# Kernel optimization log

Measured on AMD Instinct MI355X. Metric: run time of the kernel, lower is better.

The kernel has to match this reference:

```python
import jax, jax.numpy as jnp
import numpy as np

B, D, T = 4, 1024, 512      # z: [B, input_dim, T]
V, CD = 32000, 4096          # codebook: [codebook_size, codebook_dim]
EPS = 1e-12                  # F.normalize default eps


def setup_inputs() -> dict:
    key = jax.random.key(0)
    k1, k2, k3, k4 = jax.random.split(key, 4)
    z = jax.random.normal(k1, (B, D, T), dtype=jnp.float32)
    codebook = jax.random.normal(k2, (V, CD), dtype=jnp.float32) * 0.02
    cb_w = jax.random.normal(k3, (D, CD), dtype=jnp.float32) * 0.02  # torch Linear weight [out,in]
    cb_b = jax.random.normal(k4, (D,), dtype=jnp.float32) * 0.02
    return {"z": z, "codebook": codebook, "cb_w": cb_w, "cb_b": cb_b}


def _l2norm(x):
    n = jnp.sqrt(jnp.sum(x * x, axis=1, keepdims=True))
    return x / jnp.maximum(n, EPS)


def reference(z, codebook, cb_w, cb_b):
    # stride == 1, use_cblinear == True -> z_e = z
    z_e = z                                              # [B, D, T]
    proj_cb = codebook @ cb_w.T + cb_b                    # [V, D] cb_proj(codebook)

    # decode_latents
    enc = jnp.transpose(z_e, (0, 2, 1)).reshape(-1, D)    # (B*T, D)
    enc_n = _l2norm(enc)
    cb_n = _l2norm(proj_cb)
    dist = (jnp.sum(enc_n * enc_n, axis=1, keepdims=True)
            - 2.0 * enc_n @ cb_n.T
            + jnp.sum(cb_n * cb_n, axis=1)[None, :])      # (B*T, V)
    indices = jnp.argmax(-dist, axis=1).reshape(B, T)     # argmin distance
    z_q = jnp.transpose(proj_cb[indices], (0, 2, 1))      # gather un-normalized codes -> [B, D, T]

    commitment_loss = jnp.mean((z_e - jax.lax.stop_gradient(z_q)) ** 2, axis=(1, 2))  # [B]
    codebook_loss = jnp.mean((z_q - jax.lax.stop_gradient(z_e)) ** 2, axis=(1, 2))    # [B]
    z_q_st = z_e + jax.lax.stop_gradient(z_q - z_e)       # straight-through
    return z_q_st, indices, commitment_loss, codebook_loss
```

## Files before the change

### kernel.cpp

```cpp
#include <hip/hip_runtime.h>
#include <hip/hip_bf16.h>
#include <math.h>

#define B_  4
#define D_  1024
#define T_  512
#define V_  32000
#define CD_ 4096
#define NR  (B_*T_)
#define VT2 (V_/256)

typedef __attribute__((ext_vector_type(8))) short short8v;
typedef __attribute__((ext_vector_type(4))) float f32x4;

#define MFMA16(a,b,c) __builtin_amdgcn_mfma_f32_16x16x32_bf16((a),(b),(c),0,0,0)

#define ASM_VMCNT0() asm volatile("s_waitcnt vmcnt(0)" ::: "memory")
#define ASM_LGKM0()  asm volatile("s_waitcnt lgkmcnt(0)" ::: "memory")
#define SCHED_BAR()  __builtin_amdgcn_sched_barrier(0)

__device__ __forceinline__ unsigned short f2bf(float f) {
    return __builtin_bit_cast(unsigned short, __float2bfloat16(f));
}
__device__ __forceinline__ float bf2f(unsigned short u) {
    unsigned int v = ((unsigned int)u) << 16;
    return __builtin_bit_cast(float, v);
}
__device__ __forceinline__ void glds16(const unsigned short* g, unsigned short* l) {
    __builtin_amdgcn_global_load_lds(
        (const __attribute__((address_space(1))) unsigned int*)g,
        (__attribute__((address_space(3))) unsigned int*)l, 16, 0, 0);
}
__device__ __forceinline__ void cvt8(const float4& x, const float4& y,
                                     short8v& h, short8v& l) {
    float xs[8] = {x.x, x.y, x.z, x.w, y.x, y.y, y.z, y.w};
    #pragma unroll
    for (int e = 0; e < 8; ++e) {
        unsigned short hb = f2bf(xs[e]);
        h[e] = (short)hb;
        l[e] = (short)f2bf(xs[e] - bf2f(hb));
    }
}
__device__ __forceinline__ int xcd_swz(int wg, int nwg) {
    int q = nwg >> 3, r = nwg & 7;
    int x = wg & 7, o = wg >> 3;
    return (x < r ? x * (q + 1) : r * (q + 1) + (x - r) * q) + o;
}

__global__ __launch_bounds__(256) void vq_cvt(const float* __restrict__ x,
                                              unsigned short* __restrict__ hi,
                                              unsigned short* __restrict__ lo,
                                              size_t n4) {
    size_t stride = (size_t)gridDim.x * 256;
    for (size_t i = (size_t)blockIdx.x * 256 + threadIdx.x; i < n4; i += stride) {
        float4 v = *(const float4*)(x + 4 * i);
        float xs[4] = {v.x, v.y, v.z, v.w};
        ushort4 h, l;
        unsigned short* hp = (unsigned short*)&h;
        unsigned short* lp = (unsigned short*)&l;
        #pragma unroll
        for (int e = 0; e < 4; ++e) {
            hp[e] = f2bf(xs[e]);
            lp[e] = f2bf(xs[e] - bf2f(hp[e]));
        }
        *(ushort4*)(hi + 4 * i) = h;
        *(ushort4*)(lo + 4 * i) = l;
    }
}

#define T8_PHASE(pp, EXTRA)                                                   \
    {                                                                         \
        short8v aAh = *(const short8v*)&smem[cur][0][(wr8 + 2*(pp)) * 512 + lane8];     \
        short8v aAl = *(const short8v*)&smem[cur][1][(wr8 + 2*(pp)) * 512 + lane8];     \
        short8v aBh = *(const short8v*)&smem[cur][0][(wr8 + 2*(pp) + 1) * 512 + lane8]; \
        short8v aBl = *(const short8v*)&smem[cur][1][(wr8 + 2*(pp) + 1) * 512 + lane8]; \
        EXTRA;                                                                \
        SCHED_BAR();                                                          \
        __builtin_amdgcn_s_barrier();                                         \
        ASM_LGKM0();                                                          \
        SCHED_BAR();                                                          \
        __builtin_amdgcn_s_setprio(1);                                        \
        _Pragma("unroll")                                                     \
        for (int nf = 0; nf < 4; ++nf) {                                      \
            acc[2*(pp)][nf]   = MFMA16(aAh, bh[nf], acc[2*(pp)][nf]);         \
            acc[2*(pp)][nf]   = MFMA16(aAh, bl[nf], acc[2*(pp)][nf]);         \
            acc[2*(pp)][nf]   = MFMA16(aAl, bh[nf], acc[2*(pp)][nf]);         \
            acc[2*(pp)+1][nf] = MFMA16(aBh, bh[nf], acc[2*(pp)+1][nf]);       \
            acc[2*(pp)+1][nf] = MFMA16(aBh, bl[nf], acc[2*(pp)+1][nf]);       \
            acc[2*(pp)+1][nf] = MFMA16(aBl, bh[nf], acc[2*(pp)+1][nf]);       \
        }                                                                     \
        __builtin_amdgcn_s_setprio(0);                                        \
        __builtin_amdgcn_s_barrier();                                         \
        SCHED_BAR();                                                          \
    }

#define T8_CORE(KD)                                                           \
    f32x4 acc[8][4];                                                          \
    _Pragma("unroll")                                                         \
    for (int i = 0; i < 8; ++i)                                               \
        _Pragma("unroll")                                                     \
        for (int j = 0; j < 4; ++j) acc[i][j] = (f32x4){0.f, 0.f, 0.f, 0.f};  \
    const int lane = threadIdx.x & 63, w = threadIdx.x >> 6;                  \
    const int wr = w >> 2, wc = w & 3;                                        \
    const int r16 = lane & 15, kg = lane >> 4;                                \
    const int lane8 = lane * 8, wr8 = wr * 8, wc4 = wc * 4;                   \
    const int pw = w >> 1;                                                    \
    const unsigned short* gplane = (pw == 0) ? Ahp : (pw == 1) ? Alp          \
                                   : (pw == 2) ? Bhp : Blp;                   \
    const int baseRow = (pw < 2 ? mt : nt) + (w & 1) * 128 + r16;             \
    const unsigned short* gsrc = gplane + (size_t)baseRow * (KD) + kg * 8;    \
    unsigned short* lb0 = &smem[0][pw][(w & 1) * 4096 + lane8];               \
    unsigned short* lb1 = &smem[1][pw][(w & 1) * 4096 + lane8];               \
    _Pragma("unroll")                                                         \
    for (int q = 0; q < 8; ++q)                                               \
        glds16(gsrc + (size_t)q * 16 * (KD), lb0 + q * 512);                  \
    ASM_VMCNT0();                                                             \
    __builtin_amdgcn_s_barrier();                                             \
    SCHED_BAR();                                                              \
    const int NT = (KD) / 32;                                                 \
    for (int t = 0; t < NT; ++t) {                                            \
        const int cur = t & 1;                                                \
        unsigned short* lbN = cur ? lb0 : lb1;                                \
        short8v bh[4], bl[4];                                                 \
        _Pragma("unroll")                                                     \
        for (int nf = 0; nf < 4; ++nf) {                                      \
            bh[nf] = *(const short8v*)&smem[cur][2][(wc4 + nf) * 512 + lane8];\
            bl[nf] = *(const short8v*)&smem[cur][3][(wc4 + nf) * 512 + lane8];\
        }                                                                     \
        T8_PHASE(0,                                                           \
            if (t + 1 < NT) {                                                 \
                const size_t kof = (size_t)(t + 1) * 32;                      \
                _Pragma("unroll")                                             \
                for (int q = 0; q < 8; ++q)                                   \
                    glds16(gsrc + kof + (size_t)q * 16 * (KD), lbN + q * 512);\
            })                                                                \
        T8_PHASE(1, (void)0)                                                  \
        T8_PHASE(2, (void)0)                                                  \
        T8_PHASE(3, if (t + 1 < NT) { ASM_VMCNT0(); })                        \
    }

__global__ __launch_bounds__(512, 2) void vq_gemm1_t8(
    const unsigned short* __restrict__ Ahp, const unsigned short* __restrict__ Alp,
    const unsigned short* __restrict__ Bhp, const unsigned short* __restrict__ Blp,
    const float* __restrict__ bias,
    unsigned short* __restrict__ Phi, unsigned short* __restrict__ Plo)
{
    __shared__ unsigned short smem[2][4][8192];
    const int wg = xcd_swz(blockIdx.x, (V_/256) * (D_/256));
    const int mt = (wg >> 2) * 256;
    const int nt = (wg & 3) * 256;

    T8_CORE(CD_)

    #pragma unroll
    for (int nf = 0; nf < 4; ++nf) {
        const int col = nt + wc * 64 + nf * 16 + r16;
        const float bv = bias[col];
        #pragma unroll
        for (int mf = 0; mf < 8; ++mf) {
            const int rbase = mt + wr * 128 + mf * 16 + kg * 4;
            #pragma unroll
            for (int r = 0; r < 4; ++r) {
                float vv = acc[mf][nf][r] + bv;
                unsigned short h = f2bf(vv);
                unsigned short l = f2bf(vv - bf2f(h));
                size_t o = (size_t)(rbase + r) * D_ + col;
                Phi[o] = h; Plo[o] = l;
            }
        }
    }
}

__global__ __launch_bounds__(512, 2) void vq_gemm2_t8(
    const unsigned short* __restrict__ Ahp, const unsigned short* __restrict__ Alp,
    const unsigned short* __restrict__ Bhp, const unsigned short* __restrict__ Blp,
    const float* __restrict__ ninv,
    float* __restrict__ pmax, int* __restrict__ pidx)
{
    __shared__ unsigned short smem[2][4][8192];
    const int wg = xcd_swz(blockIdx.x, (NR/256) * VT2);
    const int nid = wg >> 3;
    const int mt = (wg & 7) * 256;
    const int nt = nid * 256;

    T8_CORE(D_)

    float* redv = (float*)&smem[0][0][0];
    int*   redi = (int*)&smem[0][0][2048];
    float nv[4];
    #pragma unroll
    for (int nf = 0; nf < 4; ++nf) nv[nf] = ninv[nt + wc * 64 + nf * 16 + r16];
    #pragma unroll
    for (int mf = 0; mf < 8; ++mf) {
        #pragma unroll
        for (int r = 0; r < 4; ++r) {
            float best = -INFINITY; int bi = 0x7fffffff;
            #pragma unroll
            for (int nf = 0; nf < 4; ++nf) {
                float v = acc[mf][nf][r] * nv[nf];
                int ci = nt + wc * 64 + nf * 16 + r16;
                if (v > best || (v == best && ci < bi)) { best = v; bi = ci; }
            }
            #pragma unroll
            for (int m = 8; m >= 1; m >>= 1) {
                float ov = __shfl_xor(best, m, 16);
                int   oi = __shfl_xor(bi,   m, 16);
                if (ov > best || (ov == best && oi < bi)) { best = ov; bi = oi; }
            }
            if (r16 == 0) {
                int rl = wr * 128 + mf * 16 + kg * 4 + r;
                redv[rl * 4 + wc] = best; redi[rl * 4 + wc] = bi;
            }
        }
    }
    __builtin_amdgcn_s_barrier();
    if (threadIdx.x < 256) {
        float best = -INFINITY; int bi = 0x7fffffff;
        #pragma unroll
        for (int c = 0; c < 4; ++c) {
            float v = redv[threadIdx.x * 4 + c];
            int   i = redi[threadIdx.x * 4 + c];
            if (v > best || (v == best && i < bi)) { best = v; bi = i; }
        }
        size_t o = (size_t)(mt + threadIdx.x) * VT2 + nid;
        pmax[o] = best; pidx[o] = bi;
    }
}

__global__ __launch_bounds__(256) void vq_gemm1_mfma(
    const float* __restrict__ A,
    const unsigned short* __restrict__ Bhi, const unsigned short* __restrict__ Blo,
    const float* __restrict__ bias,
    unsigned short* __restrict__ Phi, unsigned short* __restrict__ Plo)
{
    __shared__ unsigned short smem[2][4][4096];
    const int tid = threadIdx.x;
    const int lane = tid & 63, w = tid >> 6;
    const int wr = w >> 1, wc = w & 1;
    const int m_tile = blockIdx.y * 128;
    const int n_tile = blockIdx.x * 128;
    const int row16 = lane & 15, kg = lane >> 4;
    const int s0 = 2 * w, s1 = s0 + 1;
    const int lane8 = lane * 8, wr4 = wr * 4, wc4 = wc * 4;

    const float*          Ap0 = A   + (size_t)(m_tile + s0*16 + row16) * CD_ + kg*8;
    const float*          Ap1 = A   + (size_t)(m_tile + s1*16 + row16) * CD_ + kg*8;
    const unsigned short* Bp0 = Bhi + (size_t)(n_tile + s0*16 + row16) * CD_ + kg*8;
    const unsigned short* Bp1 = Bhi + (size_t)(n_tile + s1*16 + row16) * CD_ + kg*8;
    const unsigned short* Lp0 = Blo + (size_t)(n_tile + s0*16 + row16) * CD_ + kg*8;
    const unsigned short* Lp1 = Blo + (size_t)(n_tile + s1*16 + row16) * CD_ + kg*8;

    f32x4 acc[4][4];
    #pragma unroll
    for (int i = 0; i < 4; ++i)
        #pragma unroll
        for (int j = 0; j < 4; ++j) acc[i][j] = (f32x4){0.f, 0.f, 0.f, 0.f};

    float4 aw[4], al_[4];
    aw[0] = *(const float4*)(Ap0);     aw[1] = *(const float4*)(Ap0 + 4);
    aw[2] = *(const float4*)(Ap1);     aw[3] = *(const float4*)(Ap1 + 4);
    glds16(Bp0, (unsigned short*)&smem[0][2][s0*512]);
    glds16(Bp1, (unsigned short*)&smem[0][2][s1*512]);
    glds16(Lp0, (unsigned short*)&smem[0][3][s0*512]);
    glds16(Lp1, (unsigned short*)&smem[0][3][s1*512]);
    {
        short8v h0, l0, h1, l1;
        cvt8(aw[0], aw[1], h0, l0);
        cvt8(aw[2], aw[3], h1, l1);
        *(short8v*)&smem[0][0][s0*512 + lane8] = h0;
        *(short8v*)&smem[0][1][s0*512 + lane8] = l0;
        *(short8v*)&smem[0][0][s1*512 + lane8] = h1;
        *(short8v*)&smem[0][1][s1*512 + lane8] = l1;
    }
    aw[0] = *(const float4*)(Ap0 + 32); aw[1] = *(const float4*)(Ap0 + 36);
    aw[2] = *(const float4*)(Ap1 + 32); aw[3] = *(const float4*)(Ap1 + 36);
    __syncthreads();

    int cur = 0;
    const int NT = CD_ / 32;
    for (int t = 0; t < NT; ++t) {
        if (t + 1 < NT) {
            const size_t ko = (size_t)(t + 1) * 32;
            glds16(Bp0 + ko, (unsigned short*)&smem[cur^1][2][s0*512]);
            glds16(Bp1 + ko, (unsigned short*)&smem[cur^1][2][s1*512]);
            glds16(Lp0 + ko, (unsigned short*)&smem[cur^1][3][s0*512]);
            glds16(Lp1 + ko, (unsigned short*)&smem[cur^1][3][s1*512]);
            short8v h0, l0, h1, l1;
            cvt8(aw[0], aw[1], h0, l0);
            cvt8(aw[2], aw[3], h1, l1);
            *(short8v*)&smem[cur^1][0][s0*512 + lane8] = h0;
            *(short8v*)&smem[cur^1][1][s0*512 + lane8] = l0;
            *(short8v*)&smem[cur^1][0][s1*512 + lane8] = h1;
            *(short8v*)&smem[cur^1][1][s1*512 + lane8] = l1;
        }
        if (t + 2 < NT) {
            const size_t ko2 = (size_t)(t + 2) * 32;
            al_[0] = *(const float4*)(Ap0 + ko2);  al_[1] = *(const float4*)(Ap0 + ko2 + 4);
            al_[2] = *(const float4*)(Ap1 + ko2);  al_[3] = *(const float4*)(Ap1 + ko2 + 4);
        }
        short8v ah[4], av[4], bh[4], bl[4];
        #pragma unroll
        for (int f = 0; f < 4; ++f) {
            ah[f] = *(const short8v*)&smem[cur][0][(wr4+f)*512 + lane8];
            av[f] = *(const short8v*)&smem[cur][1][(wr4+f)*512 + lane8];
            bh[f] = *(const short8v*)&smem[cur][2][(wc4+f)*512 + lane8];
            bl[f] = *(const short8v*)&smem[cur][3][(wc4+f)*512 + lane8];
        }
        #pragma unroll
        for (int mf = 0; mf < 4; ++mf)
            #pragma unroll
            for (int nf = 0; nf < 4; ++nf) {
                acc[mf][nf] = MFMA16(ah[mf], bh[nf], acc[mf][nf]);
                acc[mf][nf] = MFMA16(ah[mf], bl[nf], acc[mf][nf]);
                acc[mf][nf] = MFMA16(av[mf], bh[nf], acc[mf][nf]);
            }
        __syncthreads();
        #pragma unroll
        for (int q = 0; q < 4; ++q) aw[q] = al_[q];
        cur ^= 1;
    }

    #pragma unroll
    for (int nf = 0; nf < 4; ++nf) {
        const int col = n_tile + wc*64 + nf*16 + row16;
        const float bv = bias[col];
        #pragma unroll
        for (int mf = 0; mf < 4; ++mf) {
            const int rbase = m_tile + wr*64 + mf*16 + kg*4;
            #pragma unroll
            for (int r = 0; r < 4; ++r) {
                float vv = acc[mf][nf][r] + bv;
                unsigned short h = f2bf(vv);
                unsigned short l = f2bf(vv - bf2f(h));
                size_t o = (size_t)(rbase + r) * D_ + col;
                Phi[o] = h; Plo[o] = l;
            }
        }
    }
}

__global__ __launch_bounds__(256) void vq_norms_pl(const unsigned short* __restrict__ ph,
                                                   const unsigned short* __restrict__ pl,
                                                   float* __restrict__ ninv) {
    const int row  = blockIdx.x * 4 + (threadIdx.x >> 6);
    const int lane = threadIdx.x & 63;
    float s = 0.f;
    #pragma unroll
    for (int q = 0; q < 2; ++q) {
        size_t o = (size_t)row * D_ + q * 512 + lane * 8;
        short8v h = *(const short8v*)(ph + o);
        short8v l = *(const short8v*)(pl + o);
        #pragma unroll
        for (int e = 0; e < 8; ++e) {
            float x = bf2f((unsigned short)h[e]) + bf2f((unsigned short)l[e]);
            s += x * x;
        }
    }
    #pragma unroll
    for (int off = 32; off >= 1; off >>= 1) s += __shfl_down(s, off);
    if (lane == 0) ninv[row] = 1.0f / fmaxf(sqrtf(s), 1e-12f);
}

__global__ __launch_bounds__(256) void vq_transpose_cvt(const float* __restrict__ z,
                                                        unsigned short* __restrict__ ehi,
                                                        unsigned short* __restrict__ elo) {
    __shared__ float tile[64][65];
    const int b = blockIdx.z, t0 = blockIdx.x * 64, d0 = blockIdx.y * 64;
    const int lane = threadIdx.x & 63, sub = threadIdx.x >> 6;
    for (int dd = sub; dd < 64; dd += 4)
        tile[dd][lane] = z[((size_t)b * D_ + d0 + dd) * T_ + t0 + lane];
    __syncthreads();
    for (int tt = sub; tt < 64; tt += 4) {
        float v = tile[lane][tt];
        unsigned short h = f2bf(v);
        unsigned short l = f2bf(v - bf2f(h));
        size_t o = (size_t)(b * T_ + t0 + tt) * D_ + d0 + lane;
        ehi[o] = h; elo[o] = l;
    }
}

__global__ __launch_bounds__(256) void vq_argmerge(const float* __restrict__ pmax,
                                                   const int* __restrict__ pidx,
                                                   int* __restrict__ idxw,
                                                   float* __restrict__ outI,
                                                   int vt) {
    const int i = blockIdx.x * 256 + threadIdx.x;
    if (i >= NR) return;
    float best = -INFINITY; int bi = 0;
    for (int c = 0; c < vt; c++) {
        float v = pmax[(size_t)i * vt + c];
        int   ii = pidx[(size_t)i * vt + c];
        if (v > best || (v == best && ii < bi)) { best = v; bi = ii; }
    }
    idxw[i] = bi;
    outI[i] = (float)bi;
}

__global__ __launch_bounds__(256) void vq_gather_pl(const unsigned short* __restrict__ ph,
                                                    const unsigned short* __restrict__ pl,
                                                    const int* __restrict__ idxw,
                                                    const float* __restrict__ z,
                                                    float* __restrict__ out0,
                                                    float* __restrict__ lpart) {
    __shared__ float zq[64][65];
    __shared__ int idx_s[64];
    __shared__ float wsum[4];
    const int b = blockIdx.z, t0 = blockIdx.x * 64, d0 = blockIdx.y * 64;
    const int tid = threadIdx.x;
    const int lane = tid & 63, sub = tid >> 6;
    if (tid < 64) idx_s[tid] = idxw[b * T_ + t0 + tid];
    __syncthreads();
    for (int tt = sub; tt < 64; tt += 4) {
        size_t o = (size_t)idx_s[tt] * D_ + d0 + lane;
        zq[tt][lane] = bf2f(ph[o]) + bf2f(pl[o]);
    }
    __syncthreads();
    float lacc = 0.f;
    for (int dd = sub; dd < 64; dd += 4) {
        const size_t base = ((size_t)b * D_ + d0 + dd) * T_ + t0 + lane;
        float q = zq[lane][dd];
        float zv = z[base];
        out0[base] = q;
        float dv = zv - q;
        lacc += dv * dv;
    }
    #pragma unroll
    for (int off = 32; off >= 1; off >>= 1) lacc += __shfl_down(lacc, off);
    if (lane == 0) wsum[sub] = lacc;
    __syncthreads();
    if (tid == 0)
        lpart[(blockIdx.z * 16 + blockIdx.y) * 8 + blockIdx.x] =
            wsum[0] + wsum[1] + wsum[2] + wsum[3];
}

__global__ void vq_loss(const float* __restrict__ lpart, float* __restrict__ outL) {
    const int b = threadIdx.x;
    if (b >= B_) return;
    float s = 0.f;
    for (int q = 0; q < 128; q++) s += lpart[b * 128 + q];
    s /= (float)(D_ * T_);
    outL[b]      = s;
    outL[B_ + b] = s;
}

extern "C" void kernel_launch(void* const* d_in, const int* in_sizes, int n_in,
                              void* d_out, int out_size, void* d_ws, size_t ws_size,
                              hipStream_t stream) {
    const float* z        = (const float*)d_in[0];
    const float* codebook = (const float*)d_in[1];
    const float* cb_w     = (const float*)d_in[2];
    const float* cb_b     = (const float*)d_in[3];

    float* out0 = (float*)d_out;
    float* outI = out0 + (size_t)B_*D_*T_;
    float* outL = outI + NR;

    char* p = (char*)d_ws;
    auto alloc = [&](size_t bytes) { char* r = p; p += (bytes + 255) & ~(size_t)255; return r; };
    unsigned short* w_hi = (unsigned short*)alloc((size_t)D_ * CD_ * 2);
    unsigned short* w_lo = (unsigned short*)alloc((size_t)D_ * CD_ * 2);
    unsigned short* p_hi = (unsigned short*)alloc((size_t)V_ * D_ * 2);
    unsigned short* p_lo = (unsigned short*)alloc((size_t)V_ * D_ * 2);
    unsigned short* e_hi = (unsigned short*)alloc((size_t)NR * D_ * 2);
    unsigned short* e_lo = (unsigned short*)alloc((size_t)NR * D_ * 2);
    float* ninv  = (float*)alloc((size_t)V_ * 4);
    float* pmax  = (float*)alloc((size_t)NR * VT2 * 4);
    int*   pidx  = (int*)  alloc((size_t)NR * VT2 * 4);
    int*   idxw  = (int*)  alloc((size_t)NR * 4);
    float* lpart = (float*)alloc((size_t)2048 * 4);
    unsigned short* c_hi = (unsigned short*)alloc((size_t)V_ * CD_ * 2);
    unsigned short* c_lo = (unsigned short*)alloc((size_t)V_ * CD_ * 2);
    size_t need_full = (size_t)(p - (char*)d_ws);

    vq_cvt<<<1024, 256, 0, stream>>>(cb_w, w_hi, w_lo, (size_t)D_ * CD_ / 4);
    vq_transpose_cvt<<<dim3(T_/64, D_/64, B_), 256, 0, stream>>>(z, e_hi, e_lo);

    if (ws_size >= need_full) {
        vq_cvt<<<4096, 256, 0, stream>>>(codebook, c_hi, c_lo, (size_t)V_ * CD_ / 4);
        vq_gemm1_t8<<<(V_/256) * (D_/256), 512, 0, stream>>>(c_hi, c_lo, w_hi, w_lo,
                                                             cb_b, p_hi, p_lo);
    } else {
        vq_gemm1_mfma<<<dim3(D_/128, V_/128), 256, 0, stream>>>(codebook, w_hi, w_lo,
                                                                cb_b, p_hi, p_lo);
    }
    vq_norms_pl<<<V_/4, 256, 0, stream>>>(p_hi, p_lo, ninv);
    vq_gemm2_t8<<<(NR/256) * VT2, 512, 0, stream>>>(e_hi, e_lo, p_hi, p_lo,
                                                    ninv, pmax, pidx);
    vq_argmerge<<<NR/256, 256, 0, stream>>>(pmax, pidx, idxw, outI, VT2);
    vq_gather_pl<<<dim3(T_/64, D_/64, B_), 256, 0, stream>>>(p_hi, p_lo, idxw, z,
                                                             out0, lpart);
    vq_loss<<<1, 64, 0, stream>>>(lpart, outL);
}
```

Baseline: 1.546 ms.

## Shrink both split-bf16 GEMMs to 128x128 tiles with simpler double-buffered loop

```diff
diff --git a/kernel.cpp b/kernel.cpp
--- a/kernel.cpp
+++ b/kernel.cpp
@@ -8,13 +8,14 @@
 #define V_  32000
 #define CD_ 4096
 #define NR  (B_*T_)
-#define VT2 (V_/256)
+#define VT  (V_/128)
 
 typedef __attribute__((ext_vector_type(8))) short short8v;
 typedef __attribute__((ext_vector_type(4))) float f32x4;
 
 #define MFMA16(a,b,c) __builtin_amdgcn_mfma_f32_16x16x32_bf16((a),(b),(c),0,0,0)
 
+#define ASM_VMCNT4() asm volatile("s_waitcnt vmcnt(4)" ::: "memory")
 #define ASM_VMCNT0() asm volatile("s_waitcnt vmcnt(0)" ::: "memory")
 #define ASM_LGKM0()  asm volatile("s_waitcnt lgkmcnt(0)" ::: "memory")
 #define SCHED_BAR()  __builtin_amdgcn_sched_barrier(0)
@@ -68,97 +69,102 @@
     }
 }
 
-#define T8_PHASE(pp, EXTRA)                                                   \
-    {                                                                         \
-        short8v aAh = *(const short8v*)&smem[cur][0][(wr8 + 2*(pp)) * 512 + lane8];     \
-        short8v aAl = *(const short8v*)&smem[cur][1][(wr8 + 2*(pp)) * 512 + lane8];     \
-        short8v aBh = *(const short8v*)&smem[cur][0][(wr8 + 2*(pp) + 1) * 512 + lane8]; \
-        short8v aBl = *(const short8v*)&smem[cur][1][(wr8 + 2*(pp) + 1) * 512 + lane8]; \
-        EXTRA;                                                                \
-        SCHED_BAR();                                                          \
-        __builtin_amdgcn_s_barrier();                                         \
-        ASM_LGKM0();                                                          \
-        SCHED_BAR();                                                          \
-        __builtin_amdgcn_s_setprio(1);                                        \
-        _Pragma("unroll")                                                     \
-        for (int nf = 0; nf < 4; ++nf) {                                      \
-            acc[2*(pp)][nf]   = MFMA16(aAh, bh[nf], acc[2*(pp)][nf]);         \
-            acc[2*(pp)][nf]   = MFMA16(aAh, bl[nf], acc[2*(pp)][nf]);         \
-            acc[2*(pp)][nf]   = MFMA16(aAl, bh[nf], acc[2*(pp)][nf]);         \
-            acc[2*(pp)+1][nf] = MFMA16(aBh, bh[nf], acc[2*(pp)+1][nf]);       \
-            acc[2*(pp)+1][nf] = MFMA16(aBh, bl[nf], acc[2*(pp)+1][nf]);       \
-            acc[2*(pp)+1][nf] = MFMA16(aBl, bh[nf], acc[2*(pp)+1][nf]);       \
-        }                                                                     \
-        __builtin_amdgcn_s_setprio(0);                                        \
-        __builtin_amdgcn_s_barrier();                                         \
-        SCHED_BAR();                                                          \
-    }
-
-#define T8_CORE(KD)                                                           \
-    f32x4 acc[8][4];                                                          \
+#define W128_CORE(KD)                                                         \
+    f32x4 acc[2][4];                                                          \
     _Pragma("unroll")                                                         \
-    for (int i = 0; i < 8; ++i)                                               \
+    for (int i = 0; i < 2; ++i)                                               \
         _Pragma("unroll")                                                     \
         for (int j = 0; j < 4; ++j) acc[i][j] = (f32x4){0.f, 0.f, 0.f, 0.f};  \
     const int lane = threadIdx.x & 63, w = threadIdx.x >> 6;                  \
-    const int wr = w >> 2, wc = w & 3;                                        \
+    const int wr = w >> 1, wc = w & 1;                                        \
     const int r16 = lane & 15, kg = lane >> 4;                                \
-    const int lane8 = lane * 8, wr8 = wr * 8, wc4 = wc * 4;                   \
-    const int pw = w >> 1;                                                    \
-    const unsigned short* gplane = (pw == 0) ? Ahp : (pw == 1) ? Alp          \
-                                   : (pw == 2) ? Bhp : Blp;                   \
-    const int baseRow = (pw < 2 ? mt : nt) + (w & 1) * 128 + r16;             \
-    const unsigned short* gsrc = gplane + (size_t)baseRow * (KD) + kg * 8;    \
-    unsigned short* lb0 = &smem[0][pw][(w & 1) * 4096 + lane8];               \
-    unsigned short* lb1 = &smem[1][pw][(w & 1) * 4096 + lane8];               \
+    const int lane8 = lane * 8;                                               \
+    const unsigned short* gs[4];                                              \
+    unsigned short* lds0[4];                                                  \
+    unsigned short* lds1[4];                                                  \
     _Pragma("unroll")                                                         \
-    for (int q = 0; q < 8; ++q)                                               \
-        glds16(gsrc + (size_t)q * 16 * (KD), lb0 + q * 512);                  \
+    for (int q = 0; q < 4; ++q) {                                             \
+        const int u = w * 4 + q;                                              \
+        const int pl = u >> 3, sub = u & 7;                                   \
+        const unsigned short* gp = (pl == 0) ? Ahp : (pl == 1) ? Alp          \
+                                   : (pl == 2) ? Bhp : Blp;                   \
+        const int row = ((pl < 2) ? mt : nt) + sub * 16 + r16;                \
+        gs[q] = gp + (size_t)row * (KD) + kg * 8;                             \
+        lds0[q] = &smem[0][pl][sub * 512 + lane8];                            \
+        lds1[q] = &smem[1][pl][sub * 512 + lane8];                            \
+    }                                                                         \
+    _Pragma("unroll")                                                         \
+    for (int q = 0; q < 4; ++q) glds16(gs[q], lds0[q]);                       \
     ASM_VMCNT0();                                                             \
     __builtin_amdgcn_s_barrier();                                             \
     SCHED_BAR();                                                              \
     const int NT = (KD) / 32;                                                 \
     for (int t = 0; t < NT; ++t) {                                            \
         const int cur = t & 1;                                                \
-        unsigned short* lbN = cur ? lb0 : lb1;                                \
-        short8v bh[4], bl[4];                                                 \
+        if (t + 1 < NT) {                                                     \
+            const size_t kof = (size_t)(t + 1) * 32;                          \
+            _Pragma("unroll")                                                 \
+            for (int q = 0; q < 4; ++q)                                       \
+                glds16(gs[q] + kof, cur ? lds0[q] : lds1[q]);                 \
+            ASM_VMCNT4();       \
+        } else {                                                              \
+            ASM_VMCNT0();                                                     \
+        }                                                                     \
+        __builtin_amdgcn_s_barrier();                                         \
+        SCHED_BAR();                                                          \
+        short8v ah[2], al[2], bh[4], bl[4];                                   \
+        _Pragma("unroll")                                                     \
+        for (int mf = 0; mf < 2; ++mf) {                                      \
+            ah[mf] = *(const short8v*)&smem[cur][0][(wr*2 + mf)*512 + lane8]; \
+            al[mf] = *(const short8v*)&smem[cur][1][(wr*2 + mf)*512 + lane8]; \
+        }                                                                     \
         _Pragma("unroll")                                                     \
         for (int nf = 0; nf < 4; ++nf) {                                      \
-            bh[nf] = *(const short8v*)&smem[cur][2][(wc4 + nf) * 512 + lane8];\
-            bl[nf] = *(const short8v*)&smem[cur][3][(wc4 + nf) * 512 + lane8];\
+            bh[nf] = *(const short8v*)&smem[cur][2][(wc*4 + nf)*512 + lane8]; \
+            bl[nf] = *(const short8v*)&smem[cur][3][(wc*4 + nf)*512 + lane8]; \
         }                                                                     \
-        T8_PHASE(0,                                                           \
-            if (t + 1 < NT) {                                                 \
-                const size_t kof = (size_t)(t + 1) * 32;                      \
-                _Pragma("unroll")                                             \
-                for (int q = 0; q < 8; ++q)                                   \
-                    glds16(gsrc + kof + (size_t)q * 16 * (KD), lbN + q * 512);\
-            })                                                                \
-        T8_PHASE(1, (void)0)                                                  \
-        T8_PHASE(2, (void)0)                                                  \
-        T8_PHASE(3, if (t + 1 < NT) { ASM_VMCNT0(); })                        \
-    }
-
-__global__ __launch_bounds__(512, 2) void vq_gemm1_t8(
+        __builtin_amdgcn_s_setprio(1);                                        \
+        _Pragma("unroll")                                                     \
+        for (int mf = 0; mf < 2; ++mf)                                        \
+            _Pragma("unroll")                                                 \
+            for (int nf = 0; nf < 4; ++nf)                                    \
+                acc[mf][nf] = MFMA16(ah[mf], bh[nf], acc[mf][nf]);            \
+        _Pragma("unroll")                                                     \
+        for (int mf = 0; mf < 2; ++mf)                                        \
+            _Pragma("unroll")                                                 \
+            for (int nf = 0; nf < 4; ++nf)                                    \
+                acc[mf][nf] = MFMA16(ah[mf], bl[nf], acc[mf][nf]);            \
+        _Pragma("unroll")                                                     \
+        for (int mf = 0; mf < 2; ++mf)                                        \
+            _Pragma("unroll")                                                 \
+            for (int nf = 0; nf < 4; ++nf)                                    \
+                acc[mf][nf] = MFMA16(al[mf], bh[nf], acc[mf][nf]);            \
+        __builtin_amdgcn_s_setprio(0);                                        \
+        ASM_LGKM0();                                                          \
+        __builtin_amdgcn_s_barrier();                                         \
+        SCHED_BAR();                                                          \
+    }
+
+__global__ __launch_bounds__(512, 4) void vq_gemm1_w(
     const unsigned short* __restrict__ Ahp, const unsigned short* __restrict__ Alp,
     const unsigned short* __restrict__ Bhp, const unsigned short* __restrict__ Blp,
     const float* __restrict__ bias,
     unsigned short* __restrict__ Phi, unsigned short* __restrict__ Plo)
 {
-    __shared__ unsigned short smem[2][4][8192];
-    const int wg = xcd_swz(blockIdx.x, (V_/256) * (D_/256));
-    const int mt = (wg >> 2) * 256;
-    const int nt = (wg & 3) * 256;
-
-    T8_CORE(CD_)
+    __shared__ unsigned short smem[2][4][4096];
+    const int wg = xcd_swz(blockIdx.x, VT * (D_/128));
+    const int mt = (wg >> 3) * 128;
+    const int nt = (wg & 7) * 128;
+
+    W128_CORE(CD_)
 
     #pragma unroll
     for (int nf = 0; nf < 4; ++nf) {
         const int col = nt + wc * 64 + nf * 16 + r16;
         const float bv = bias[col];
         #pragma unroll
-        for (int mf = 0; mf < 8; ++mf) {
-            const int rbase = mt + wr * 128 + mf * 16 + kg * 4;
+        for (int mf = 0; mf < 2; ++mf) {
+            const int rbase = mt + wr * 32 + mf * 16 + kg * 4;
             #pragma unroll
             for (int r = 0; r < 4; ++r) {
                 float vv = acc[mf][nf][r] + bv;
@@ -171,27 +177,27 @@
     }
 }
 
-__global__ __launch_bounds__(512, 2) void vq_gemm2_t8(
+__global__ __launch_bounds__(512, 4) void vq_gemm2_w(
     const unsigned short* __restrict__ Ahp, const unsigned short* __restrict__ Alp,
     const unsigned short* __restrict__ Bhp, const unsigned short* __restrict__ Blp,
     const float* __restrict__ ninv,
     float* __restrict__ pmax, int* __restrict__ pidx)
 {
-    __shared__ unsigned short smem[2][4][8192];
-    const int wg = xcd_swz(blockIdx.x, (NR/256) * VT2);
-    const int nid = wg >> 3;
-    const int mt = (wg & 7) * 256;
-    const int nt = nid * 256;
-
-    T8_CORE(D_)
+    __shared__ unsigned short smem[2][4][4096];
+    const int wg = xcd_swz(blockIdx.x, (NR/128) * VT);
+    const int nid = wg >> 4;
+    const int mt = (wg & 15) * 128;
+    const int nt = nid * 128;
+
+    W128_CORE(D_)
 
     float* redv = (float*)&smem[0][0][0];
-    int*   redi = (int*)&smem[0][0][2048];
+    int*   redi = (int*)&smem[0][0][1024];
     float nv[4];
     #pragma unroll
     for (int nf = 0; nf < 4; ++nf) nv[nf] = ninv[nt + wc * 64 + nf * 16 + r16];
     #pragma unroll
-    for (int mf = 0; mf < 8; ++mf) {
+    for (int mf = 0; mf < 2; ++mf) {
         #pragma unroll
         for (int r = 0; r < 4; ++r) {
             float best = -INFINITY; int bi = 0x7fffffff;
@@ -208,22 +214,19 @@
                 if (ov > best || (ov == best && oi < bi)) { best = ov; bi = oi; }
             }
             if (r16 == 0) {
-                int rl = wr * 128 + mf * 16 + kg * 4 + r;
-                redv[rl * 4 + wc] = best; redi[rl * 4 + wc] = bi;
+                int rl = wr * 32 + mf * 16 + kg * 4 + r;
+                redv[wc * 128 + rl] = best; redi[wc * 128 + rl] = bi;
             }
         }
     }
     __builtin_amdgcn_s_barrier();
-    if (threadIdx.x < 256) {
-        float best = -INFINITY; int bi = 0x7fffffff;
-        #pragma unroll
-        for (int c = 0; c < 4; ++c) {
-            float v = redv[threadIdx.x * 4 + c];
-            int   i = redi[threadIdx.x * 4 + c];
-            if (v > best || (v == best && i < bi)) { best = v; bi = i; }
-        }
-        size_t o = (size_t)(mt + threadIdx.x) * VT2 + nid;
-        pmax[o] = best; pidx[o] = bi;
+    if (threadIdx.x < 128) {
+        float v0 = redv[threadIdx.x],       v1 = redv[128 + threadIdx.x];
+        int   i0 = redi[threadIdx.x],       i1 = redi[128 + threadIdx.x];
+        bool t1 = (v1 > v0) || (v1 == v0 && i1 < i0);
+        size_t o = (size_t)(mt + threadIdx.x) * VT + nid;
+        pmax[o] = t1 ? v1 : v0;
+        pidx[o] = t1 ? i1 : i0;
     }
 }
 
@@ -464,8 +467,8 @@
     unsigned short* e_hi = (unsigned short*)alloc((size_t)NR * D_ * 2);
     unsigned short* e_lo = (unsigned short*)alloc((size_t)NR * D_ * 2);
     float* ninv  = (float*)alloc((size_t)V_ * 4);
-    float* pmax  = (float*)alloc((size_t)NR * VT2 * 4);
-    int*   pidx  = (int*)  alloc((size_t)NR * VT2 * 4);
+    float* pmax  = (float*)alloc((size_t)NR * VT * 4);
+    int*   pidx  = (int*)  alloc((size_t)NR * VT * 4);
     int*   idxw  = (int*)  alloc((size_t)NR * 4);
     float* lpart = (float*)alloc((size_t)2048 * 4);
     unsigned short* c_hi = (unsigned short*)alloc((size_t)V_ * CD_ * 2);
@@ -477,16 +480,16 @@
 
     if (ws_size >= need_full) {
         vq_cvt<<<4096, 256, 0, stream>>>(codebook, c_hi, c_lo, (size_t)V_ * CD_ / 4);
-        vq_gemm1_t8<<<(V_/256) * (D_/256), 512, 0, stream>>>(c_hi, c_lo, w_hi, w_lo,
-                                                             cb_b, p_hi, p_lo);
+        vq_gemm1_w<<<VT * (D_/128), 512, 0, stream>>>(c_hi, c_lo, w_hi, w_lo,
+                                                      cb_b, p_hi, p_lo);
     } else {
         vq_gemm1_mfma<<<dim3(D_/128, V_/128), 256, 0, stream>>>(codebook, w_hi, w_lo,
                                                                 cb_b, p_hi, p_lo);
     }
     vq_norms_pl<<<V_/4, 256, 0, stream>>>(p_hi, p_lo, ninv);
-    vq_gemm2_t8<<<(NR/256) * VT2, 512, 0, stream>>>(e_hi, e_lo, p_hi, p_lo,
-                                                    ninv, pmax, pidx);
-    vq_argmerge<<<NR/256, 256, 0, stream>>>(pmax, pidx, idxw, outI, VT2);
+    vq_gemm2_w<<<(NR/128) * VT, 512, 0, stream>>>(e_hi, e_lo, p_hi, p_lo,
+                                                  ninv, pmax, pidx);
+    vq_argmerge<<<NR/256, 256, 0, stream>>>(pmax, pidx, idxw, outI, VT);
     vq_gather_pl<<<dim3(T_/64, D_/64, B_), 256, 0, stream>>>(p_hi, p_lo, idxw, z,
                                                              out0, lpart);
     vq_loss<<<1, 64, 0, stream>>>(lpart, outL);
```

Measured after the change: 1.796 ms. +16.2%, slower.

## Fuse codebook fp32-to-bf16 split into projection GEMM via direct fp32 LDS staging

Applied to the files above, without the earlier changes.

```diff
diff --git a/kernel.cpp b/kernel.cpp
--- a/kernel.cpp
+++ b/kernel.cpp
@@ -15,6 +15,7 @@
 
 #define MFMA16(a,b,c) __builtin_amdgcn_mfma_f32_16x16x32_bf16((a),(b),(c),0,0,0)
 
+#define ASM_VMCNT8() asm volatile("s_waitcnt vmcnt(8)" ::: "memory")
 #define ASM_VMCNT0() asm volatile("s_waitcnt vmcnt(0)" ::: "memory")
 #define ASM_LGKM0()  asm volatile("s_waitcnt lgkmcnt(0)" ::: "memory")
 #define SCHED_BAR()  __builtin_amdgcn_sched_barrier(0)
@@ -27,6 +28,11 @@
     return __builtin_bit_cast(float, v);
 }
 __device__ __forceinline__ void glds16(const unsigned short* g, unsigned short* l) {
+    __builtin_amdgcn_global_load_lds(
+        (const __attribute__((address_space(1))) unsigned int*)g,
+        (__attribute__((address_space(3))) unsigned int*)l, 16, 0, 0);
+}
+__device__ __forceinline__ void gldsf(const float* g, float* l) {
     __builtin_amdgcn_global_load_lds(
         (const __attribute__((address_space(1))) unsigned int*)g,
         (__attribute__((address_space(3))) unsigned int*)l, 16, 0, 0);
@@ -65,6 +71,123 @@
         }
         *(ushort4*)(hi + 4 * i) = h;
         *(ushort4*)(lo + 4 * i) = l;
+    }
+}
+
+__global__ __launch_bounds__(512, 2) void vq_gemm1_f(
+    const float* __restrict__ Acb,
+    const unsigned short* __restrict__ Bhp, const unsigned short* __restrict__ Blp,
+    const float* __restrict__ bias,
+    unsigned short* __restrict__ Phi, unsigned short* __restrict__ Plo)
+{
+    __shared__ float          Af[2][8192];
+    __shared__ unsigned short Bh[2][8192];
+    __shared__ unsigned short Bl[2][8192];
+    const int wg = xcd_swz(blockIdx.x, (V_/256) * (D_/256));
+    const int mt = (wg >> 2) * 256;
+    const int nt = (wg & 3) * 256;
+    const int lane = threadIdx.x & 63, w = threadIdx.x >> 6;
+    const int wr = w >> 2, wc = w & 3;
+    const int r16 = lane & 15, kg = lane >> 4;
+    const int lane8 = lane * 8, wr8 = wr * 8, wc4 = wc * 4;
+
+    f32x4 acc[8][4];
+    #pragma unroll
+    for (int i = 0; i < 8; ++i)
+        #pragma unroll
+        for (int j = 0; j < 4; ++j) acc[i][j] = (f32x4){0.f, 0.f, 0.f, 0.f};
+
+#define STAGE1F(b, kk) do {                                                   \
+    if (w < 4) {                                                              \
+        _Pragma("unroll")                                                     \
+        for (int j = 0; j < 4; ++j) {                                         \
+            const int sub = w * 4 + j;                                        \
+            const float* g0 = Acb + (size_t)(mt + sub*16 + r16) * CD_         \
+                              + (kk) + kg * 4;                                \
+            gldsf(g0,      &Af[b][sub*512]);                                  \
+            gldsf(g0 + 16, &Af[b][sub*512 + 256]);                            \
+        }                                                                     \
+    } else if (w < 6) {                                                       \
+        const int sb = (w - 4) * 8;                                           \
+        _Pragma("unroll")                                                     \
+        for (int j = 0; j < 8; ++j)                                           \
+            glds16(Bhp + (size_t)(nt + (sb+j)*16 + r16) * CD_ + (kk) + kg*8,  \
+                   &Bh[b][(sb+j)*512]);                                       \
+    } else {                                                                  \
+        const int sb = (w - 6) * 8;                                           \
+        _Pragma("unroll")                                                     \
+        for (int j = 0; j < 8; ++j)                                           \
+            glds16(Blp + (size_t)(nt + (sb+j)*16 + r16) * CD_ + (kk) + kg*8,  \
+                   &Bl[b][(sb+j)*512]);                                       \
+    }                                                                         \
+} while (0)
+
+    STAGE1F(0, 0);
+    ASM_VMCNT0();
+    __builtin_amdgcn_s_barrier();
+    SCHED_BAR();
+
+    const int NT = CD_ / 32;
+    const int afrag = (kg >> 1) * 256 + (kg & 1) * 128 + r16 * 4;
+    for (int t = 0; t < NT; ++t) {
+        const int cur = t & 1;
+        if (t + 1 < NT) {
+            STAGE1F(cur ^ 1, (size_t)(t + 1) * 32);
+            ASM_VMCNT8();
+        } else {
+            ASM_VMCNT0();
+        }
+        __builtin_amdgcn_s_barrier();
+        SCHED_BAR();
+        short8v bh[4], bl[4];
+        #pragma unroll
+        for (int nf = 0; nf < 4; ++nf) {
+            bh[nf] = *(const short8v*)&Bh[cur][(wc4 + nf) * 512 + lane8];
+            bl[nf] = *(const short8v*)&Bl[cur][(wc4 + nf) * 512 + lane8];
+        }
+        #pragma unroll
+        for (int g = 0; g < 4; ++g) {
+            const float* f0 = &Af[cur][(wr8 + 2*g) * 512 + afrag];
+            const float* f1 = &Af[cur][(wr8 + 2*g + 1) * 512 + afrag];
+            float4 x0 = *(const float4*)f0, x1 = *(const float4*)(f0 + 64);
+            float4 y0 = *(const float4*)f1, y1 = *(const float4*)(f1 + 64);
+            short8v a0h, a0l, a1h, a1l;
+            cvt8(x0, x1, a0h, a0l);
+            cvt8(y0, y1, a1h, a1l);
+            __builtin_amdgcn_s_setprio(1);
+            #pragma unroll
+            for (int nf = 0; nf < 4; ++nf) {
+                acc[2*g][nf]   = MFMA16(a0h, bh[nf], acc[2*g][nf]);
+                acc[2*g][nf]   = MFMA16(a0h, bl[nf], acc[2*g][nf]);
+                acc[2*g][nf]   = MFMA16(a0l, bh[nf], acc[2*g][nf]);
+                acc[2*g+1][nf] = MFMA16(a1h, bh[nf], acc[2*g+1][nf]);
+                acc[2*g+1][nf] = MFMA16(a1h, bl[nf], acc[2*g+1][nf]);
+                acc[2*g+1][nf] = MFMA16(a1l, bh[nf], acc[2*g+1][nf]);
+            }
+            __builtin_amdgcn_s_setprio(0);
+        }
+        ASM_LGKM0();
+        __builtin_amdgcn_s_barrier();
+        SCHED_BAR();
+    }
+#undef STAGE1F
+
+    #pragma unroll
+    for (int nf = 0; nf < 4; ++nf) {
+        const int col = nt + wc * 64 + nf * 16 + r16;
+        const float bv = bias[col];
+        #pragma unroll
+        for (int mf = 0; mf < 8; ++mf) {
+            const int rbase = mt + wr * 128 + mf * 16 + kg * 4;
+            #pragma unroll
+            for (int r = 0; r < 4; ++r) {
+                float vv = acc[mf][nf][r] + bv;
+                unsigned short h = f2bf(vv);
+                unsigned short l = f2bf(vv - bf2f(h));
+                size_t o = (size_t)(rbase + r) * D_ + col;
+                Phi[o] = h; Plo[o] = l;
+            }
+        }
     }
 }
 
@@ -94,83 +217,6 @@
         SCHED_BAR();                                                          \
     }
 
-#define T8_CORE(KD)                                                           \
-    f32x4 acc[8][4];                                                          \
-    _Pragma("unroll")                                                         \
-    for (int i = 0; i < 8; ++i)                                               \
-        _Pragma("unroll")                                                     \
-        for (int j = 0; j < 4; ++j) acc[i][j] = (f32x4){0.f, 0.f, 0.f, 0.f};  \
-    const int lane = threadIdx.x & 63, w = threadIdx.x >> 6;                  \
-    const int wr = w >> 2, wc = w & 3;                                        \
-    const int r16 = lane & 15, kg = lane >> 4;                                \
-    const int lane8 = lane * 8, wr8 = wr * 8, wc4 = wc * 4;                   \
-    const int pw = w >> 1;                                                    \
-    const unsigned short* gplane = (pw == 0) ? Ahp : (pw == 1) ? Alp          \
-                                   : (pw == 2) ? Bhp : Blp;                   \
-    const int baseRow = (pw < 2 ? mt : nt) + (w & 1) * 128 + r16;             \
-    const unsigned short* gsrc = gplane + (size_t)baseRow * (KD) + kg * 8;    \
-    unsigned short* lb0 = &smem[0][pw][(w & 1) * 4096 + lane8];               \
-    unsigned short* lb1 = &smem[1][pw][(w & 1) * 4096 + lane8];               \
-    _Pragma("unroll")                                                         \
-    for (int q = 0; q < 8; ++q)                                               \
-        glds16(gsrc + (size_t)q * 16 * (KD), lb0 + q * 512);                  \
-    ASM_VMCNT0();                                                             \
-    __builtin_amdgcn_s_barrier();                                             \
-    SCHED_BAR();                                                              \
-    const int NT = (KD) / 32;                                                 \
-    for (int t = 0; t < NT; ++t) {                                            \
-        const int cur = t & 1;                                                \
-        unsigned short* lbN = cur ? lb0 : lb1;                                \
-        short8v bh[4], bl[4];                                                 \
-        _Pragma("unroll")                                                     \
-        for (int nf = 0; nf < 4; ++nf) {                                      \
-            bh[nf] = *(const short8v*)&smem[cur][2][(wc4 + nf) * 512 + lane8];\
-            bl[nf] = *(const short8v*)&smem[cur][3][(wc4 + nf) * 512 + lane8];\
-        }                                                                     \
-        T8_PHASE(0,                                                           \
-            if (t + 1 < NT) {                                                 \
-                const size_t kof = (size_t)(t + 1) * 32;                      \
-                _Pragma("unroll")                                             \
-                for (int q = 0; q < 8; ++q)                                   \
-                    glds16(gsrc + kof + (size_t)q * 16 * (KD), lbN + q * 512);\
-            })                                                                \
-        T8_PHASE(1, (void)0)                                                  \
-        T8_PHASE(2, (void)0)                                                  \
-        T8_PHASE(3, if (t + 1 < NT) { ASM_VMCNT0(); })                        \
-    }
-
-__global__ __launch_bounds__(512, 2) void vq_gemm1_t8(
-    const unsigned short* __restrict__ Ahp, const unsigned short* __restrict__ Alp,
-    const unsigned short* __restrict__ Bhp, const unsigned short* __restrict__ Blp,
-    const float* __restrict__ bias,
-    unsigned short* __restrict__ Phi, unsigned short* __restrict__ Plo)
-{
-    __shared__ unsigned short smem[2][4][8192];
-    const int wg = xcd_swz(blockIdx.x, (V_/256) * (D_/256));
-    const int mt = (wg >> 2) * 256;
-    const int nt = (wg & 3) * 256;
-
-    T8_CORE(CD_)
-
-    #pragma unroll
-    for (int nf = 0; nf < 4; ++nf) {
-        const int col = nt + wc * 64 + nf * 16 + r16;
-        const float bv = bias[col];
-        #pragma unroll
-        for (int mf = 0; mf < 8; ++mf) {
-            const int rbase = mt + wr * 128 + mf * 16 + kg * 4;
-            #pragma unroll
-            for (int r = 0; r < 4; ++r) {
-                float vv = acc[mf][nf][r] + bv;
-                unsigned short h = f2bf(vv);
-                unsigned short l = f2bf(vv - bf2f(h));
-                size_t o = (size_t)(rbase + r) * D_ + col;
-                Phi[o] = h; Plo[o] = l;
-            }
-        }
-    }
-}
-
 __global__ __launch_bounds__(512, 2) void vq_gemm2_t8(
     const unsigned short* __restrict__ Ahp, const unsigned short* __restrict__ Alp,
     const unsigned short* __restrict__ Bhp, const unsigned short* __restrict__ Blp,
@@ -183,7 +229,49 @@
     const int mt = (wg & 7) * 256;
     const int nt = nid * 256;
 
-    T8_CORE(D_)
+    f32x4 acc[8][4];
+    #pragma unroll
+    for (int i = 0; i < 8; ++i)
+        #pragma unroll
+        for (int j = 0; j < 4; ++j) acc[i][j] = (f32x4){0.f, 0.f, 0.f, 0.f};
+    const int lane = threadIdx.x & 63, w = threadIdx.x >> 6;
+    const int wr = w >> 2, wc = w & 3;
+    const int r16 = lane & 15, kg = lane >> 4;
+    const int lane8 = lane * 8, wr8 = wr * 8, wc4 = wc * 4;
+    const int pw = w >> 1;
+    const unsigned short* gplane = (pw == 0) ? Ahp : (pw == 1) ? Alp
+                                   : (pw == 2) ? Bhp : Blp;
+    const int baseRow = (pw < 2 ? mt : nt) + (w & 1) * 128 + r16;
+    const unsigned short* gsrc = gplane + (size_t)baseRow * D_ + kg * 8;
+    unsigned short* lb0 = &smem[0][pw][(w & 1) * 4096 + lane8];
+    unsigned short* lb1 = &smem[1][pw][(w & 1) * 4096 + lane8];
+    #pragma unroll
+    for (int q = 0; q < 8; ++q)
+        glds16(gsrc + (size_t)q * 16 * D_, lb0 + q * 512);
+    ASM_VMCNT0();
+    __builtin_amdgcn_s_barrier();
+    SCHED_BAR();
+    const int NT = D_ / 32;
+    for (int t = 0; t < NT; ++t) {
+        const int cur = t & 1;
+        unsigned short* lbN = cur ? lb0 : lb1;
+        short8v bh[4], bl[4];
+        #pragma unroll
+        for (int nf = 0; nf < 4; ++nf) {
+            bh[nf] = *(const short8v*)&smem[cur][2][(wc4 + nf) * 512 + lane8];
+            bl[nf] = *(const short8v*)&smem[cur][3][(wc4 + nf) * 512 + lane8];
+        }
+        T8_PHASE(0,
+            if (t + 1 < NT) {
+                const size_t kof = (size_t)(t + 1) * 32;
+                _Pragma("unroll")
+                for (int q = 0; q < 8; ++q)
+                    glds16(gsrc + kof + (size_t)q * 16 * D_, lbN + q * 512);
+            })
+        T8_PHASE(1, (void)0)
+        T8_PHASE(2, (void)0)
+        T8_PHASE(3, if (t + 1 < NT) { ASM_VMCNT0(); })
+    }
 
     float* redv = (float*)&smem[0][0][0];
     int*   redi = (int*)&smem[0][0][2048];
@@ -227,118 +315,6 @@
     }
 }
 
-__global__ __launch_bounds__(256) void vq_gemm1_mfma(
-    const float* __restrict__ A,
-    const unsigned short* __restrict__ Bhi, const unsigned short* __restrict__ Blo,
-    const float* __restrict__ bias,
-    unsigned short* __restrict__ Phi, unsigned short* __restrict__ Plo)
-{
-    __shared__ unsigned short smem[2][4][4096];
-    const int tid = threadIdx.x;
-    const int lane = tid & 63, w = tid >> 6;
-    const int wr = w >> 1, wc = w & 1;
-    const int m_tile = blockIdx.y * 128;
-    const int n_tile = blockIdx.x * 128;
-    const int row16 = lane & 15, kg = lane >> 4;
-    const int s0 = 2 * w, s1 = s0 + 1;
-    const int lane8 = lane * 8, wr4 = wr * 4, wc4 = wc * 4;
-
-    const float*          Ap0 = A   + (size_t)(m_tile + s0*16 + row16) * CD_ + kg*8;
-    const float*          Ap1 = A   + (size_t)(m_tile + s1*16 + row16) * CD_ + kg*8;
-    const unsigned short* Bp0 = Bhi + (size_t)(n_tile + s0*16 + row16) * CD_ + kg*8;
-    const unsigned short* Bp1 = Bhi + (size_t)(n_tile + s1*16 + row16) * CD_ + kg*8;
-    const unsigned short* Lp0 = Blo + (size_t)(n_tile + s0*16 + row16) * CD_ + kg*8;
-    const unsigned short* Lp1 = Blo + (size_t)(n_tile + s1*16 + row16) * CD_ + kg*8;
-
-    f32x4 acc[4][4];
-    #pragma unroll
-    for (int i = 0; i < 4; ++i)
-        #pragma unroll
-        for (int j = 0; j < 4; ++j) acc[i][j] = (f32x4){0.f, 0.f, 0.f, 0.f};
-
-    float4 aw[4], al_[4];
-    aw[0] = *(const float4*)(Ap0);     aw[1] = *(const float4*)(Ap0 + 4);
-    aw[2] = *(const float4*)(Ap1);     aw[3] = *(const float4*)(Ap1 + 4);
-    glds16(Bp0, (unsigned short*)&smem[0][2][s0*512]);
-    glds16(Bp1, (unsigned short*)&smem[0][2][s1*512]);
-    glds16(Lp0, (unsigned short*)&smem[0][3][s0*512]);
-    glds16(Lp1, (unsigned short*)&smem[0][3][s1*512]);
-    {
-        short8v h0, l0, h1, l1;
-        cvt8(aw[0], aw[1], h0, l0);
-        cvt8(aw[2], aw[3], h1, l1);
-        *(short8v*)&smem[0][0][s0*512 + lane8] = h0;
-        *(short8v*)&smem[0][1][s0*512 + lane8] = l0;
-        *(short8v*)&smem[0][0][s1*512 + lane8] = h1;
-        *(short8v*)&smem[0][1][s1*512 + lane8] = l1;
-    }
-    aw[0] = *(const float4*)(Ap0 + 32); aw[1] = *(const float4*)(Ap0 + 36);
-    aw[2] = *(const float4*)(Ap1 + 32); aw[3] = *(const float4*)(Ap1 + 36);
-    __syncthreads();
-
-    int cur = 0;
-    const int NT = CD_ / 32;
-    for (int t = 0; t < NT; ++t) {
-        if (t + 1 < NT) {
-            const size_t ko = (size_t)(t + 1) * 32;
-            glds16(Bp0 + ko, (unsigned short*)&smem[cur^1][2][s0*512]);
-            glds16(Bp1 + ko, (unsigned short*)&smem[cur^1][2][s1*512]);
-            glds16(Lp0 + ko, (unsigned short*)&smem[cur^1][3][s0*512]);
-            glds16(Lp1 + ko, (unsigned short*)&smem[cur^1][3][s1*512]);
-            short8v h0, l0, h1, l1;
-            cvt8(aw[0], aw[1], h0, l0);
-            cvt8(aw[2], aw[3], h1, l1);
-            *(short8v*)&smem[cur^1][0][s0*512 + lane8] = h0;
-            *(short8v*)&smem[cur^1][1][s0*512 + lane8] = l0;
-            *(short8v*)&smem[cur^1][0][s1*512 + lane8] = h1;
-            *(short8v*)&smem[cur^1][1][s1*512 + lane8] = l1;
-        }
-        if (t + 2 < NT) {
-            const size_t ko2 = (size_t)(t + 2) * 32;
-            al_[0] = *(const float4*)(Ap0 + ko2);  al_[1] = *(const float4*)(Ap0 + ko2 + 4);
-            al_[2] = *(const float4*)(Ap1 + ko2);  al_[3] = *(const float4*)(Ap1 + ko2 + 4);
-        }
-        short8v ah[4], av[4], bh[4], bl[4];
-        #pragma unroll
-        for (int f = 0; f < 4; ++f) {
-            ah[f] = *(const short8v*)&smem[cur][0][(wr4+f)*512 + lane8];
-            av[f] = *(const short8v*)&smem[cur][1][(wr4+f)*512 + lane8];
-            bh[f] = *(const short8v*)&smem[cur][2][(wc4+f)*512 + lane8];
-            bl[f] = *(const short8v*)&smem[cur][3][(wc4+f)*512 + lane8];
-        }
-        #pragma unroll
-        for (int mf = 0; mf < 4; ++mf)
-            #pragma unroll
-            for (int nf = 0; nf < 4; ++nf) {
-                acc[mf][nf] = MFMA16(ah[mf], bh[nf], acc[mf][nf]);
-                acc[mf][nf] = MFMA16(ah[mf], bl[nf], acc[mf][nf]);
-                acc[mf][nf] = MFMA16(av[mf], bh[nf], acc[mf][nf]);
-            }
-        __syncthreads();
-        #pragma unroll
-        for (int q = 0; q < 4; ++q) aw[q] = al_[q];
-        cur ^= 1;
-    }
-
-    #pragma unroll
-    for (int nf = 0; nf < 4; ++nf) {
-        const int col = n_tile + wc*64 + nf*16 + row16;
-        const float bv = bias[col];
-        #pragma unroll
-        for (int mf = 0; mf < 4; ++mf) {
-            const int rbase = m_tile + wr*64 + mf*16 + kg*4;
-            #pragma unroll
-            for (int r = 0; r < 4; ++r) {
-                float vv = acc[mf][nf][r] + bv;
-                unsigned short h = f2bf(vv);
-                unsigned short l = f2bf(vv - bf2f(h));
-                size_t o = (size_t)(rbase + r) * D_ + col;
-                Phi[o] = h; Plo[o] = l;
-            }
-        }
-    }
-}
-
 __global__ __launch_bounds__(256) void vq_norms_pl(const unsigned short* __restrict__ ph,
                                                    const unsigned short* __restrict__ pl,
                                                    float* __restrict__ ninv) {
@@ -468,21 +444,12 @@
     int*   pidx  = (int*)  alloc((size_t)NR * VT2 * 4);
     int*   idxw  = (int*)  alloc((size_t)NR * 4);
     float* lpart = (float*)alloc((size_t)2048 * 4);
-    unsigned short* c_hi = (unsigned short*)alloc((size_t)V_ * CD_ * 2);
-    unsigned short* c_lo = (unsigned short*)alloc((size_t)V_ * CD_ * 2);
-    size_t need_full = (size_t)(p - (char*)d_ws);
-
-    vq_cvt<<<1024, 256, 0, stream>>>(cb_w, w_hi, w_lo, (size_t)D_ * CD_ / 4);
+
+    vq_cvt<<<512, 256, 0, stream>>>(cb_w, w_hi, w_lo, (size_t)D_ * CD_ / 4);
     vq_transpose_cvt<<<dim3(T_/64, D_/64, B_), 256, 0, stream>>>(z, e_hi, e_lo);
 
-    if (ws_size >= need_full) {
-        vq_cvt<<<4096, 256, 0, stream>>>(codebook, c_hi, c_lo, (size_t)V_ * CD_ / 4);
-        vq_gemm1_t8<<<(V_/256) * (D_/256), 512, 0, stream>>>(c_hi, c_lo, w_hi, w_lo,
-                                                             cb_b, p_hi, p_lo);
-    } else {
-        vq_gemm1_mfma<<<dim3(D_/128, V_/128), 256, 0, stream>>>(codebook, w_hi, w_lo,
-                                                                cb_b, p_hi, p_lo);
-    }
+    vq_gemm1_f<<<(V_/256) * (D_/256), 512, 0, stream>>>(codebook, w_hi, w_lo,
+                                                        cb_b, p_hi, p_lo);
     vq_norms_pl<<<V_/4, 256, 0, stream>>>(p_hi, p_lo, ninv);
     vq_gemm2_t8<<<(NR/256) * VT2, 512, 0, stream>>>(e_hi, e_lo, p_hi, p_lo,
                                                     ninv, pmax, pidx);
```

Result: no change. 1.573 ms (+1.8%).
